# Kernel optimization log

Hardware: AMD Instinct MI355X
Metric: run time of the kernel (lower is better)

Reference implementation:

```python
import jax, jax.numpy as jnp
import numpy as np

N_NODES = 100_000
N_EDGES = 1_600_000
HIDDEN = 256
N_LAYERS = 5
N_GRAPHS = 256
NUM_ATOM_TYPE = 120
NUM_CHIRALITY = 3
NUM_BOND_TYPE = 6
NUM_BOND_DIR = 3


def setup_inputs() -> dict:
    key = jax.random.key(0)
    ks = jax.random.split(key, 16)
    x = jax.random.randint(ks[0], (N_NODES, 2), 0, 3)
    edge_index = jax.random.randint(ks[1], (2, N_EDGES), 0, N_NODES)
    edge_attr = jax.random.randint(ks[2], (N_EDGES, 2), 0, 3)
    batch = jnp.sort(jax.random.randint(ks[3], (N_NODES,), 0, N_GRAPHS))
    # embedding tables (xavier-uniform-ish scale)
    def emb(k, n, d):
        a = np.sqrt(6.0 / (n + d))
        return jax.random.uniform(k, (n, d), jnp.float32, -a, a)
    xe1 = emb(ks[4], NUM_ATOM_TYPE, HIDDEN)
    xe2 = emb(ks[5], NUM_CHIRALITY, HIDDEN)
    ee1 = emb(ks[6], NUM_BOND_TYPE, HIDDEN)
    ee2 = emb(ks[7], NUM_BOND_DIR, HIDDEN)
    s = 1.0 / np.sqrt(HIDDEN)
    W1 = jax.random.uniform(ks[8], (N_LAYERS, HIDDEN, HIDDEN), jnp.float32, -s, s)
    b1 = jax.random.uniform(ks[9], (N_LAYERS, HIDDEN), jnp.float32, -s, s)
    W2 = jax.random.uniform(ks[10], (N_LAYERS, HIDDEN, HIDDEN), jnp.float32, -s, s)
    b2 = jax.random.uniform(ks[11], (N_LAYERS, HIDDEN), jnp.float32, -s, s)
    return {"x": x, "edge_index": edge_index, "edge_attr": edge_attr, "batch": batch,
            "xe1": xe1, "xe2": xe2, "ee1": ee1, "ee2": ee2,
            "W1": W1, "b1": b1, "W2": W2, "b2": b2}


def reference(x, edge_index, edge_attr, batch, xe1, xe2, ee1, ee2, W1, b1, W2, b2):
    # node / edge input embeddings (sum of two lookups)
    z = xe1[x[:, 0]] + xe2[x[:, 1]]                      # [N, H]
    e = ee1[edge_attr[:, 0]] + ee2[edge_attr[:, 1]]      # [E, H]
    src, dst = edge_index[0], edge_index[1]
    for l in range(N_LAYERS):
        # GINEConv: nn((1+eps)*x_i + sum_j relu(x_j + e_ij)), eps = 0
        msg = jax.nn.relu(z[src] + e)                    # [E, H]
        agg = jax.ops.segment_sum(msg, dst, num_segments=N_NODES)
        h = z + agg                                      # (1+0)*x + aggr
        h = jax.nn.relu(h @ W1[l] + b1[l]) @ W2[l] + b2[l]
        z = jax.nn.relu(h)                               # outer relu in GIN.forward
    # global mean pool over graphs
    sums = jax.ops.segment_sum(z, batch, num_segments=N_GRAPHS)      # [G, H]
    cnts = jax.ops.segment_sum(jnp.ones((z.shape[0], 1), z.dtype), batch, num_segments=N_GRAPHS)
    g = sums / jnp.maximum(cnts, 1.0)
    # dropout p=0.0 -> identity
    return (z, g)
```

## Files before the change

kernel.cpp:

```cpp
#include <hip/hip_runtime.h>
#include <hip/hip_bf16.h>

#define HID 256
#define NCODES 18
#define SCAN_CHUNK 2048
#define LROW 264

typedef _Float16 h8_t __attribute__((ext_vector_type(8)));
typedef _Float16 h4_t __attribute__((ext_vector_type(4)));
typedef float f4_t __attribute__((ext_vector_type(4)));

__global__ void etab_kernel(const float* __restrict__ ee1, const float* __restrict__ ee2,
                            _Float16* __restrict__ etab) {
    int t = blockIdx.x;
    int c = threadIdx.x;
    etab[t * HID + c] = (_Float16)(ee1[(t / 3) * HID + c] + ee2[(t % 3) * HID + c]);
}

__global__ __launch_bounds__(256) void embed_kernel(const int* __restrict__ x,
                                                    const float* __restrict__ xe1,
                                                    const float* __restrict__ xe2,
                                                    _Float16* __restrict__ zh, int N) {
    int node = blockIdx.x * 4 + (threadIdx.x >> 6);
    int lane = threadIdx.x & 63;
    if (node >= N) return;
    int a0 = x[node * 2 + 0];
    int a1 = x[node * 2 + 1];
    const float4 u = *(const float4*)(xe1 + (size_t)a0 * HID + lane * 4);
    const float4 v = *(const float4*)(xe2 + (size_t)a1 * HID + lane * 4);
    h4_t r;
    r.x = (_Float16)(u.x + v.x); r.y = (_Float16)(u.y + v.y);
    r.z = (_Float16)(u.z + v.z); r.w = (_Float16)(u.w + v.w);
    *(h4_t*)(zh + (size_t)node * HID + lane * 4) = r;
}

__global__ __launch_bounds__(256) void prep_w(const float* __restrict__ W,
                                              _Float16* __restrict__ Wt) {
    __shared__ float t[32][33];
    int m = blockIdx.z;
    int tx = threadIdx.x & 31, ty = threadIdx.x >> 5;
    const float* Wm = W + (size_t)m * HID * HID;
    _Float16* Wtm = Wt + (size_t)m * HID * HID;
    int k0 = blockIdx.x * 32, n0 = blockIdx.y * 32;
#pragma unroll
    for (int j = 0; j < 4; ++j) { int r = ty + j * 8; t[r][tx] = Wm[(k0 + r) * HID + n0 + tx]; }
    __syncthreads();
#pragma unroll
    for (int j = 0; j < 4; ++j) { int r = ty + j * 8; Wtm[(size_t)(n0 + r) * HID + k0 + tx] = (_Float16)t[tx][r]; }
}

__global__ void hist_kernel(const int* __restrict__ ei, int E, int* __restrict__ deg) {
    int i = blockIdx.x * 256 + threadIdx.x;
    if (i < E) atomicAdd(&deg[ei[E + i]], 1);
}

__global__ __launch_bounds__(256) void scan_partial(const int* __restrict__ deg, int n,
                                                    int* __restrict__ psum) {
    __shared__ int red[256];
    int base = blockIdx.x * SCAN_CHUNK;
    int s = 0;
    for (int i = threadIdx.x; i < SCAN_CHUNK; i += 256) {
        int idx = base + i;
        if (idx < n) s += deg[idx];
    }
    red[threadIdx.x] = s;
    __syncthreads();
    for (int off = 128; off > 0; off >>= 1) {
        if (threadIdx.x < off) red[threadIdx.x] += red[threadIdx.x + off];
        __syncthreads();
    }
    if (threadIdx.x == 0) psum[blockIdx.x] = red[0];
}

__global__ void scan_sums(int* psum, int nchunks) {
    if (blockIdx.x == 0 && threadIdx.x == 0) {
        int acc = 0;
        for (int i = 0; i < nchunks; i++) { int v = psum[i]; psum[i] = acc; acc += v; }
    }
}

__global__ __launch_bounds__(256) void scan_apply(const int* __restrict__ deg, int n,
                                                  const int* __restrict__ psum,
                                                  int* __restrict__ row_start,
                                                  int* __restrict__ cursor, int E) {
    __shared__ int tmp[256];
    int tid = threadIdx.x;
    int base = blockIdx.x * SCAN_CHUNK;
    int tb = base + tid * 8;
    int loc[8];
    int s = 0;
    for (int j = 0; j < 8; j++) {
        loc[j] = s;
        int idx = tb + j;
        if (idx < n) s += deg[idx];
    }
    tmp[tid] = s;
    __syncthreads();
    for (int off = 1; off < 256; off <<= 1) {
        int v = 0;
        if (tid >= off) v = tmp[tid - off];
        __syncthreads();
        if (tid >= off) tmp[tid] += v;
        __syncthreads();
    }
    int excl = tmp[tid] - s + psum[blockIdx.x];
    for (int j = 0; j < 8; j++) {
        int idx = tb + j;
        if (idx < n) {
            int v = excl + loc[j];
            row_start[idx] = v;
            cursor[idx] = v;
        }
    }
    if (blockIdx.x == 0 && tid == 0) row_start[n] = E;
}

__global__ void fill_kernel(const int* __restrict__ ei, const int* __restrict__ ea, int E,
                            int* __restrict__ cursor, unsigned* __restrict__ csr) {
    int i = blockIdx.x * 256 + threadIdx.x;
    if (i >= E) return;
    int dst = ei[E + i];
    int src = ei[i];
    int code = ea[i * 2] * 3 + ea[i * 2 + 1];
    int p = atomicAdd(&cursor[dst], 1);
    csr[p] = (unsigned)src | ((unsigned)code << 20);
}

__global__ __launch_bounds__(256) void agg_kernel(const _Float16* __restrict__ zh,
                                                  const int* __restrict__ row_start,
                                                  const unsigned* __restrict__ csr,
                                                  const _Float16* __restrict__ etab,
                                                  _Float16* __restrict__ h0h, int N) {
    int tid = threadIdx.x;
    int node = blockIdx.x * 8 + (tid >> 5);
    int l32 = tid & 31;
    if (node >= N) return;
    h8_t self = *(const h8_t*)(zh + (size_t)node * HID + l32 * 8);
    float acc[8];
#pragma unroll
    for (int j = 0; j < 8; ++j) acc[j] = (float)self[j];
    int s = row_start[node];
    int e = row_start[node + 1];
    int i = s;
    for (; i + 2 <= e; i += 2) {
        unsigned p0 = csr[i], p1 = csr[i + 1];
        h8_t z0 = *(const h8_t*)(zh + (size_t)(p0 & 0xFFFFF) * HID + l32 * 8);
        h8_t e0 = *(const h8_t*)(etab + (size_t)(p0 >> 20) * HID + l32 * 8);
        h8_t z1 = *(const h8_t*)(zh + (size_t)(p1 & 0xFFFFF) * HID + l32 * 8);
        h8_t e1 = *(const h8_t*)(etab + (size_t)(p1 >> 20) * HID + l32 * 8);
#pragma unroll
        for (int j = 0; j < 8; ++j) {
            acc[j] += fmaxf((float)z0[j] + (float)e0[j], 0.f);
            acc[j] += fmaxf((float)z1[j] + (float)e1[j], 0.f);
        }
    }
    if (i < e) {
        unsigned p0 = csr[i];
        h8_t z0 = *(const h8_t*)(zh + (size_t)(p0 & 0xFFFFF) * HID + l32 * 8);
        h8_t e0 = *(const h8_t*)(etab + (size_t)(p0 >> 20) * HID + l32 * 8);
#pragma unroll
        for (int j = 0; j < 8; ++j) acc[j] += fmaxf((float)z0[j] + (float)e0[j], 0.f);
    }
    h8_t o;
#pragma unroll
    for (int j = 0; j < 8; ++j) o[j] = (_Float16)acc[j];
    *(h8_t*)(h0h + (size_t)node * HID + l32 * 8) = o;
}

__global__ __launch_bounds__(256, 2) void mlp_fused(const _Float16* __restrict__ A,
                                                    const _Float16* __restrict__ Wt1,
                                                    const float* __restrict__ b1,
                                                    const _Float16* __restrict__ Wt2,
                                                    const float* __restrict__ b2,
                                                    _Float16* __restrict__ outh,
                                                    float* __restrict__ outf,
                                                    int M, int writef) {
    __shared__ _Float16 As[64 * LROW];
    __shared__ _Float16 Ys[64 * LROW];
    int tid = threadIdx.x;
    int lane = tid & 63;
    int w = tid >> 6;
    int row0 = blockIdx.x * 64;
    const _Float16* Ab = A + (size_t)row0 * HID;

#pragma unroll
    for (int it = 0; it < 8; ++it) {
        int c = it * 256 + tid;
        int row = c >> 5, cir = c & 31;
        h8_t v = *(const h8_t*)(Ab + row * HID + cir * 8);
        *(h8_t*)(As + row * LROW + cir * 8) = v;
    }
    __syncthreads();

    int wc = w * 64;
    int l16 = lane & 15;
    int lq = lane >> 4;

    {
        f4_t acc[4][4] = {};
#pragma unroll
        for (int ks = 0; ks < 8; ++ks) {
            h8_t a[4], b[4];
#pragma unroll
            for (int mi = 0; mi < 4; ++mi)
                a[mi] = *(const h8_t*)(As + (mi * 16 + l16) * LROW + (ks * 4 + lq) * 8);
#pragma unroll
            for (int ni = 0; ni < 4; ++ni)
                b[ni] = *(const h8_t*)(Wt1 + (size_t)(wc + ni * 16 + l16) * HID + ks * 32 + lq * 8);
#pragma unroll
            for (int mi = 0; mi < 4; ++mi)
#pragma unroll
                for (int ni = 0; ni < 4; ++ni)
                    acc[mi][ni] = __builtin_amdgcn_mfma_f32_16x16x32_f16(a[mi], b[ni], acc[mi][ni], 0, 0, 0);
        }
#pragma unroll
        for (int ni = 0; ni < 4; ++ni) {
            int col = wc + ni * 16 + l16;
            float bv = b1[col];
#pragma unroll
            for (int mi = 0; mi < 4; ++mi)
#pragma unroll
                for (int r = 0; r < 4; ++r) {
                    int rr = mi * 16 + lq * 4 + r;
                    Ys[rr * LROW + col] = (_Float16)fmaxf(acc[mi][ni][r] + bv, 0.f);
                }
        }
    }
    __syncthreads();

    {
        f4_t acc[4][4] = {};
#pragma unroll
        for (int ks = 0; ks < 8; ++ks) {
            h8_t a[4], b[4];
#pragma unroll
            for (int mi = 0; mi < 4; ++mi)
                a[mi] = *(const h8_t*)(Ys + (mi * 16 + l16) * LROW + (ks * 4 + lq) * 8);
#pragma unroll
            for (int ni = 0; ni < 4; ++ni)
                b[ni] = *(const h8_t*)(Wt2 + (size_t)(wc + ni * 16 + l16) * HID + ks * 32 + lq * 8);
#pragma unroll
            for (int mi = 0; mi < 4; ++mi)
#pragma unroll
                for (int ni = 0; ni < 4; ++ni)
                    acc[mi][ni] = __builtin_amdgcn_mfma_f32_16x16x32_f16(a[mi], b[ni], acc[mi][ni], 0, 0, 0);
        }
#pragma unroll
        for (int ni = 0; ni < 4; ++ni) {
            int col = wc + ni * 16 + l16;
            float bv = b2[col];
#pragma unroll
            for (int mi = 0; mi < 4; ++mi)
#pragma unroll
                for (int r = 0; r < 4; ++r) {
                    int rr = mi * 16 + lq * 4 + r;
                    As[rr * LROW + col] = (_Float16)fmaxf(acc[mi][ni][r] + bv, 0.f);
                }
        }
    }
    __syncthreads();

#pragma unroll
    for (int it = 0; it < 8; ++it) {
        int c = it * 256 + tid;
        int row = c >> 5, cir = c & 31;
        int grow = row0 + row;
        if (grow < M) {
            h8_t v = *(const h8_t*)(As + row * LROW + cir * 8);
            *(h8_t*)(outh + (size_t)grow * HID + cir * 8) = v;
            if (writef) {
                f4_t f0, f1;
#pragma unroll
                for (int j = 0; j < 4; ++j) { f0[j] = (float)v[j]; f1[j] = (float)v[j + 4]; }
                *(f4_t*)(outf + (size_t)grow * HID + cir * 8) = f0;
                *(f4_t*)(outf + (size_t)grow * HID + cir * 8 + 4) = f1;
            }
        }
    }
}

__global__ __launch_bounds__(1024) void pool_kernel(const _Float16* __restrict__ zh,
                                                    const int* __restrict__ batch, int N,
                                                    float* __restrict__ g) {
    __shared__ float red[32 * 32 * 8];
    int gid = blockIdx.x;
    int lo = 0, hi = N;
    while (lo < hi) { int mid = (lo + hi) >> 1; if (batch[mid] < gid) lo = mid + 1; else hi = mid; }
    int start = lo;
    int lo2 = start, hi2 = N;
    while (lo2 < hi2) { int mid = (lo2 + hi2) >> 1; if (batch[mid] < gid + 1) lo2 = mid + 1; else hi2 = mid; }
    int end = lo2;
    int cnt = end - start;

    int r = threadIdx.x >> 5;
    int ch = threadIdx.x & 31;
    float acc[8] = {};
    for (int row = start + r; row < end; row += 32) {
        h8_t v = *(const h8_t*)(zh + (size_t)row * HID + ch * 8);
#pragma unroll
        for (int j = 0; j < 8; ++j) acc[j] += (float)v[j];
    }
    float* slot = red + (r * 32 + ch) * 8;
#pragma unroll
    for (int j = 0; j < 8; ++j) slot[j] = acc[j];
    __syncthreads();
    for (int off = 16; off > 0; off >>= 1) {
        if (r < off) {
            const float* o = red + ((r + off) * 32 + ch) * 8;
#pragma unroll
            for (int j = 0; j < 8; ++j) { acc[j] += o[j]; slot[j] = acc[j]; }
        }
        __syncthreads();
    }
    if (r == 0) {
        float inv = 1.0f / fmaxf((float)cnt, 1.0f);
#pragma unroll
        for (int j = 0; j < 8; ++j) g[(size_t)gid * HID + ch * 8 + j] = acc[j] * inv;
    }
}

extern "C" void kernel_launch(void* const* d_in, const int* in_sizes, int n_in,
                              void* d_out, int out_size, void* d_ws, size_t ws_size,
                              hipStream_t stream) {
    const int* x = (const int*)d_in[0];
    const int* ei = (const int*)d_in[1];
    const int* ea = (const int*)d_in[2];
    const int* batch = (const int*)d_in[3];
    const float* xe1 = (const float*)d_in[4];
    const float* xe2 = (const float*)d_in[5];
    const float* ee1 = (const float*)d_in[6];
    const float* ee2 = (const float*)d_in[7];
    const float* W1 = (const float*)d_in[8];
    const float* b1 = (const float*)d_in[9];
    const float* W2 = (const float*)d_in[10];
    const float* b2 = (const float*)d_in[11];

    int N = in_sizes[0] / 2;
    int E = in_sizes[1] / 2;
    int G = out_size / HID - N;
    int Np = ((N + 127) / 128) * 128;
    int nbm = (N + 63) / 64;

    float* z = (float*)d_out;
    float* gout = z + (size_t)N * HID;

    char* w = (char*)d_ws;
    _Float16* h0h = (_Float16*)w;  w += (size_t)Np * HID * 2;
    _Float16* zh  = (_Float16*)w;  w += (size_t)Np * HID * 2;
    _Float16* Wt1 = (_Float16*)w;  w += (size_t)5 * HID * HID * 2;
    _Float16* Wt2 = (_Float16*)w;  w += (size_t)5 * HID * HID * 2;
    _Float16* etabh = (_Float16*)w; w += (size_t)NCODES * HID * 2;
    int* deg = (int*)w;       w += (size_t)N * 4;
    int* row_start = (int*)w; w += (size_t)(N + 1) * 4;
    int* cursor = (int*)w;    w += (size_t)N * 4;
    int* psum = (int*)w;      w += 64 * 4;
    unsigned* csr = (unsigned*)w;

    hipMemsetAsync(deg, 0, (size_t)N * 4, stream);
    etab_kernel<<<NCODES, HID, 0, stream>>>(ee1, ee2, etabh);
    embed_kernel<<<(N + 3) / 4, 256, 0, stream>>>(x, xe1, xe2, zh, N);
    prep_w<<<dim3(8, 8, 5), 256, 0, stream>>>(W1, Wt1);
    prep_w<<<dim3(8, 8, 5), 256, 0, stream>>>(W2, Wt2);
    hist_kernel<<<(E + 255) / 256, 256, 0, stream>>>(ei, E, deg);
    int nchunks = (N + SCAN_CHUNK - 1) / SCAN_CHUNK;
    scan_partial<<<nchunks, 256, 0, stream>>>(deg, N, psum);
    scan_sums<<<1, 1, 0, stream>>>(psum, nchunks);
    scan_apply<<<nchunks, 256, 0, stream>>>(deg, N, psum, row_start, cursor, E);
    fill_kernel<<<(E + 255) / 256, 256, 0, stream>>>(ei, ea, E, cursor, csr);

    for (int l = 0; l < 5; l++) {
        agg_kernel<<<(N + 7) / 8, 256, 0, stream>>>(zh, row_start, csr, etabh, h0h, N);
        mlp_fused<<<nbm, 256, 0, stream>>>(h0h, Wt1 + (size_t)l * HID * HID,
                                           b1 + (size_t)l * HID,
                                           Wt2 + (size_t)l * HID * HID,
                                           b2 + (size_t)l * HID,
                                           zh, z, N, (l == 4) ? 1 : 0);
    }
    pool_kernel<<<G, 1024, 0, stream>>>(zh, batch, N, gout);
}
```

Baseline: 1.280 ms.

## Bucket CSR build, LDS edge table with packed-half aggregation, 512-thread MLP

CSR construction now runs in two passes: edges are first scattered into 128-node buckets, then each bucket is placed into the final CSR by one block, which localizes the per-destination atomics and writes. The aggregation kernel caches the 18-entry edge-embedding table in shared memory, processes four nodes per half-wave with 4-way unrolled gathers, and does the add and relu in packed fp16 before accumulating in fp32. The MLP kernel moves to 512 threads with eight waves splitting both rows and columns, plus an extra barrier before overwriting As. The risks are reduced precision from summing four fp16 messages before the fp32 accumulate, and the packing limits src to 17 bits and code to 5 bits.

```diff
diff --git a/kernel.cpp b/kernel.cpp
--- a/kernel.cpp
+++ b/kernel.cpp
@@ -5,6 +5,7 @@
 #define NCODES 18
 #define SCAN_CHUNK 2048
 #define LROW 264
+#define BSH 7
 
 typedef _Float16 h8_t __attribute__((ext_vector_type(8)));
 typedef _Float16 h4_t __attribute__((ext_vector_type(4)));
@@ -115,15 +116,39 @@
     if (blockIdx.x == 0 && tid == 0) row_start[n] = E;
 }
 
-__global__ void fill_kernel(const int* __restrict__ ei, const int* __restrict__ ea, int E,
-                            int* __restrict__ cursor, unsigned* __restrict__ csr) {
+__global__ void init_bcur(const int* __restrict__ row_start, int* __restrict__ bcur, int nb) {
+    int b = blockIdx.x * 256 + threadIdx.x;
+    if (b < nb) bcur[b] = row_start[b << BSH];
+}
+
+__global__ void bucket_scatter(const int* __restrict__ ei, const int* __restrict__ ea, int E,
+                               int* __restrict__ bcur, unsigned* __restrict__ tmp) {
     int i = blockIdx.x * 256 + threadIdx.x;
     if (i >= E) return;
     int dst = ei[E + i];
     int src = ei[i];
     int code = ea[i * 2] * 3 + ea[i * 2 + 1];
-    int p = atomicAdd(&cursor[dst], 1);
-    csr[p] = (unsigned)src | ((unsigned)code << 20);
+    int b = dst >> BSH;
+    int p = atomicAdd(&bcur[b], 1);
+    tmp[p] = (unsigned)src | ((unsigned)code << 17) | ((unsigned)(dst & 127) << 22);
+}
+
+__global__ __launch_bounds__(256) void bucket_fill(const int* __restrict__ row_start,
+                                                   const unsigned* __restrict__ tmp,
+                                                   int* __restrict__ cursor,
+                                                   unsigned* __restrict__ csr, int N) {
+    int b = blockIdx.x;
+    int lo = b << BSH;
+    int hi = lo + (1 << BSH);
+    if (hi > N) hi = N;
+    int base = row_start[lo];
+    int cnt = row_start[hi] - base;
+    for (int i = threadIdx.x; i < cnt; i += 256) {
+        unsigned e = tmp[base + i];
+        int dst = lo + ((e >> 22) & 127);
+        int pos = atomicAdd(&cursor[dst], 1);
+        csr[pos] = (e & 0x1FFFF) | (((e >> 17) & 31) << 20);
+    }
 }
 
 __global__ __launch_bounds__(256) void agg_kernel(const _Float16* __restrict__ zh,
@@ -131,50 +156,69 @@
                                                   const unsigned* __restrict__ csr,
                                                   const _Float16* __restrict__ etab,
                                                   _Float16* __restrict__ h0h, int N) {
+    __shared__ _Float16 et[NCODES * HID];
     int tid = threadIdx.x;
-    int node = blockIdx.x * 8 + (tid >> 5);
+    for (int c = tid; c < NCODES * 32; c += 256)
+        *(h8_t*)(et + c * 8) = *(const h8_t*)(etab + c * 8);
+    __syncthreads();
+
+    int w = tid >> 6;
     int l32 = tid & 31;
-    if (node >= N) return;
-    h8_t self = *(const h8_t*)(zh + (size_t)node * HID + l32 * 8);
-    float acc[8];
-#pragma unroll
-    for (int j = 0; j < 8; ++j) acc[j] = (float)self[j];
-    int s = row_start[node];
-    int e = row_start[node + 1];
-    int i = s;
-    for (; i + 2 <= e; i += 2) {
-        unsigned p0 = csr[i], p1 = csr[i + 1];
-        h8_t z0 = *(const h8_t*)(zh + (size_t)(p0 & 0xFFFFF) * HID + l32 * 8);
-        h8_t e0 = *(const h8_t*)(etab + (size_t)(p0 >> 20) * HID + l32 * 8);
-        h8_t z1 = *(const h8_t*)(zh + (size_t)(p1 & 0xFFFFF) * HID + l32 * 8);
-        h8_t e1 = *(const h8_t*)(etab + (size_t)(p1 >> 20) * HID + l32 * 8);
-#pragma unroll
-        for (int j = 0; j < 8; ++j) {
-            acc[j] += fmaxf((float)z0[j] + (float)e0[j], 0.f);
-            acc[j] += fmaxf((float)z1[j] + (float)e1[j], 0.f);
-        }
-    }
-    if (i < e) {
-        unsigned p0 = csr[i];
-        h8_t z0 = *(const h8_t*)(zh + (size_t)(p0 & 0xFFFFF) * HID + l32 * 8);
-        h8_t e0 = *(const h8_t*)(etab + (size_t)(p0 >> 20) * HID + l32 * 8);
-#pragma unroll
-        for (int j = 0; j < 8; ++j) acc[j] += fmaxf((float)z0[j] + (float)e0[j], 0.f);
-    }
-    h8_t o;
-#pragma unroll
-    for (int j = 0; j < 8; ++j) o[j] = (_Float16)acc[j];
-    *(h8_t*)(h0h + (size_t)node * HID + l32 * 8) = o;
-}
-
-__global__ __launch_bounds__(256, 2) void mlp_fused(const _Float16* __restrict__ A,
-                                                    const _Float16* __restrict__ Wt1,
-                                                    const float* __restrict__ b1,
-                                                    const _Float16* __restrict__ Wt2,
-                                                    const float* __restrict__ b2,
-                                                    _Float16* __restrict__ outh,
-                                                    float* __restrict__ outf,
-                                                    int M, int writef) {
+    int half = (tid >> 5) & 1;
+    int base = blockIdx.x * 32 + w * 8;
+    const h8_t hz = {};
+
+    for (int t = 0; t < 4; ++t) {
+        int node = base + t * 2 + half;
+        if (node >= N) continue;
+        h8_t self = *(const h8_t*)(zh + (size_t)node * HID + l32 * 8);
+        float acc[8];
+#pragma unroll
+        for (int j = 0; j < 8; ++j) acc[j] = (float)self[j];
+        int s = row_start[node];
+        int e = row_start[node + 1];
+        int i = s;
+        for (; i + 4 <= e; i += 4) {
+            unsigned p0 = csr[i], p1 = csr[i + 1], p2 = csr[i + 2], p3 = csr[i + 3];
+            h8_t z0 = *(const h8_t*)(zh + (size_t)(p0 & 0xFFFFF) * HID + l32 * 8);
+            h8_t z1 = *(const h8_t*)(zh + (size_t)(p1 & 0xFFFFF) * HID + l32 * 8);
+            h8_t z2 = *(const h8_t*)(zh + (size_t)(p2 & 0xFFFFF) * HID + l32 * 8);
+            h8_t z3 = *(const h8_t*)(zh + (size_t)(p3 & 0xFFFFF) * HID + l32 * 8);
+            h8_t e0 = *(const h8_t*)(et + (p0 >> 20) * HID + l32 * 8);
+            h8_t e1 = *(const h8_t*)(et + (p1 >> 20) * HID + l32 * 8);
+            h8_t e2 = *(const h8_t*)(et + (p2 >> 20) * HID + l32 * 8);
+            h8_t e3 = *(const h8_t*)(et + (p3 >> 20) * HID + l32 * 8);
+            h8_t m0 = __builtin_elementwise_max(z0 + e0, hz);
+            h8_t m1 = __builtin_elementwise_max(z1 + e1, hz);
+            h8_t m2 = __builtin_elementwise_max(z2 + e2, hz);
+            h8_t m3 = __builtin_elementwise_max(z3 + e3, hz);
+            h8_t sm = (m0 + m1) + (m2 + m3);
+#pragma unroll
+            for (int j = 0; j < 8; ++j) acc[j] += (float)sm[j];
+        }
+        for (; i < e; ++i) {
+            unsigned p0 = csr[i];
+            h8_t z0 = *(const h8_t*)(zh + (size_t)(p0 & 0xFFFFF) * HID + l32 * 8);
+            h8_t e0 = *(const h8_t*)(et + (p0 >> 20) * HID + l32 * 8);
+            h8_t m0 = __builtin_elementwise_max(z0 + e0, hz);
+#pragma unroll
+            for (int j = 0; j < 8; ++j) acc[j] += (float)m0[j];
+        }
+        h8_t o;
+#pragma unroll
+        for (int j = 0; j < 8; ++j) o[j] = (_Float16)acc[j];
+        *(h8_t*)(h0h + (size_t)node * HID + l32 * 8) = o;
+    }
+}
+
+__global__ __launch_bounds__(512, 4) void mlp_kernel(const _Float16* __restrict__ A,
+                                                     const _Float16* __restrict__ Wt1,
+                                                     const float* __restrict__ b1,
+                                                     const _Float16* __restrict__ Wt2,
+                                                     const float* __restrict__ b2,
+                                                     _Float16* __restrict__ outh,
+                                                     float* __restrict__ outf,
+                                                     int M, int writef) {
     __shared__ _Float16 As[64 * LROW];
     __shared__ _Float16 Ys[64 * LROW];
     int tid = threadIdx.x;
@@ -184,31 +228,31 @@
     const _Float16* Ab = A + (size_t)row0 * HID;
 
 #pragma unroll
-    for (int it = 0; it < 8; ++it) {
-        int c = it * 256 + tid;
+    for (int it = 0; it < 4; ++it) {
+        int c = it * 512 + tid;
         int row = c >> 5, cir = c & 31;
-        h8_t v = *(const h8_t*)(Ab + row * HID + cir * 8);
-        *(h8_t*)(As + row * LROW + cir * 8) = v;
-    }
-    __syncthreads();
-
-    int wc = w * 64;
+        *(h8_t*)(As + row * LROW + cir * 8) = *(const h8_t*)(Ab + row * HID + cir * 8);
+    }
+    __syncthreads();
+
+    int mh = (w >> 2) * 32;
+    int wc = (w & 3) * 64;
     int l16 = lane & 15;
     int lq = lane >> 4;
 
     {
-        f4_t acc[4][4] = {};
+        f4_t acc[2][4] = {};
 #pragma unroll
         for (int ks = 0; ks < 8; ++ks) {
-            h8_t a[4], b[4];
-#pragma unroll
-            for (int mi = 0; mi < 4; ++mi)
-                a[mi] = *(const h8_t*)(As + (mi * 16 + l16) * LROW + (ks * 4 + lq) * 8);
+            h8_t a[2], b[4];
+#pragma unroll
+            for (int mi = 0; mi < 2; ++mi)
+                a[mi] = *(const h8_t*)(As + (mh + mi * 16 + l16) * LROW + (ks * 4 + lq) * 8);
 #pragma unroll
             for (int ni = 0; ni < 4; ++ni)
                 b[ni] = *(const h8_t*)(Wt1 + (size_t)(wc + ni * 16 + l16) * HID + ks * 32 + lq * 8);
 #pragma unroll
-            for (int mi = 0; mi < 4; ++mi)
+            for (int mi = 0; mi < 2; ++mi)
 #pragma unroll
                 for (int ni = 0; ni < 4; ++ni)
                     acc[mi][ni] = __builtin_amdgcn_mfma_f32_16x16x32_f16(a[mi], b[ni], acc[mi][ni], 0, 0, 0);
@@ -218,10 +262,10 @@
             int col = wc + ni * 16 + l16;
             float bv = b1[col];
 #pragma unroll
-            for (int mi = 0; mi < 4; ++mi)
+            for (int mi = 0; mi < 2; ++mi)
 #pragma unroll
                 for (int r = 0; r < 4; ++r) {
-                    int rr = mi * 16 + lq * 4 + r;
+                    int rr = mh + mi * 16 + lq * 4 + r;
                     Ys[rr * LROW + col] = (_Float16)fmaxf(acc[mi][ni][r] + bv, 0.f);
                 }
         }
@@ -229,31 +273,32 @@
     __syncthreads();
 
     {
-        f4_t acc[4][4] = {};
+        f4_t acc[2][4] = {};
 #pragma unroll
         for (int ks = 0; ks < 8; ++ks) {
-            h8_t a[4], b[4];
-#pragma unroll
-            for (int mi = 0; mi < 4; ++mi)
-                a[mi] = *(const h8_t*)(Ys + (mi * 16 + l16) * LROW + (ks * 4 + lq) * 8);
+            h8_t a[2], b[4];
+#pragma unroll
+            for (int mi = 0; mi < 2; ++mi)
+                a[mi] = *(const h8_t*)(Ys + (mh + mi * 16 + l16) * LROW + (ks * 4 + lq) * 8);
 #pragma unroll
             for (int ni = 0; ni < 4; ++ni)
                 b[ni] = *(const h8_t*)(Wt2 + (size_t)(wc + ni * 16 + l16) * HID + ks * 32 + lq * 8);
 #pragma unroll
-            for (int mi = 0; mi < 4; ++mi)
+            for (int mi = 0; mi < 2; ++mi)
 #pragma unroll
                 for (int ni = 0; ni < 4; ++ni)
                     acc[mi][ni] = __builtin_amdgcn_mfma_f32_16x16x32_f16(a[mi], b[ni], acc[mi][ni], 0, 0, 0);
         }
+        __syncthreads();
 #pragma unroll
         for (int ni = 0; ni < 4; ++ni) {
             int col = wc + ni * 16 + l16;
             float bv = b2[col];
 #pragma unroll
-            for (int mi = 0; mi < 4; ++mi)
+            for (int mi = 0; mi < 2; ++mi)
 #pragma unroll
                 for (int r = 0; r < 4; ++r) {
-                    int rr = mi * 16 + lq * 4 + r;
+                    int rr = mh + mi * 16 + lq * 4 + r;
                     As[rr * LROW + col] = (_Float16)fmaxf(acc[mi][ni][r] + bv, 0.f);
                 }
         }
@@ -261,8 +306,8 @@
     __syncthreads();
 
 #pragma unroll
-    for (int it = 0; it < 8; ++it) {
-        int c = it * 256 + tid;
+    for (int it = 0; it < 4; ++it) {
+        int c = it * 512 + tid;
         int row = c >> 5, cir = c & 31;
         int grow = row0 + row;
         if (grow < M) {
@@ -338,8 +383,9 @@
     int N = in_sizes[0] / 2;
     int E = in_sizes[1] / 2;
     int G = out_size / HID - N;
-    int Np = ((N + 127) / 128) * 128;
     int nbm = (N + 63) / 64;
+    int Np = nbm * 64;
+    int nb = (N + (1 << BSH) - 1) >> BSH;
 
     float* z = (float*)d_out;
     float* gout = z + (size_t)N * HID;
@@ -354,7 +400,9 @@
     int* row_start = (int*)w; w += (size_t)(N + 1) * 4;
     int* cursor = (int*)w;    w += (size_t)N * 4;
     int* psum = (int*)w;      w += 64 * 4;
-    unsigned* csr = (unsigned*)w;
+    int* bcur = (int*)w;      w += 1024 * 4;
+    unsigned* csr = (unsigned*)w; w += (size_t)E * 4;
+    unsigned* tmp = (unsigned*)w;
 
     hipMemsetAsync(deg, 0, (size_t)N * 4, stream);
     etab_kernel<<<NCODES, HID, 0, stream>>>(ee1, ee2, etabh);
@@ -366,15 +414,17 @@
     scan_partial<<<nchunks, 256, 0, stream>>>(deg, N, psum);
     scan_sums<<<1, 1, 0, stream>>>(psum, nchunks);
     scan_apply<<<nchunks, 256, 0, stream>>>(deg, N, psum, row_start, cursor, E);
-    fill_kernel<<<(E + 255) / 256, 256, 0, stream>>>(ei, ea, E, cursor, csr);
+    init_bcur<<<(nb + 255) / 256, 256, 0, stream>>>(row_start, bcur, nb);
+    bucket_scatter<<<(E + 255) / 256, 256, 0, stream>>>(ei, ea, E, bcur, tmp);
+    bucket_fill<<<nb, 256, 0, stream>>>(row_start, tmp, cursor, csr, N);
 
     for (int l = 0; l < 5; l++) {
-        agg_kernel<<<(N + 7) / 8, 256, 0, stream>>>(zh, row_start, csr, etabh, h0h, N);
-        mlp_fused<<<nbm, 256, 0, stream>>>(h0h, Wt1 + (size_t)l * HID * HID,
-                                           b1 + (size_t)l * HID,
-                                           Wt2 + (size_t)l * HID * HID,
-                                           b2 + (size_t)l * HID,
-                                           zh, z, N, (l == 4) ? 1 : 0);
+        agg_kernel<<<(N + 31) / 32, 256, 0, stream>>>(zh, row_start, csr, etabh, h0h, N);
+        mlp_kernel<<<nbm, 512, 0, stream>>>(h0h, Wt1 + (size_t)l * HID * HID,
+                                            b1 + (size_t)l * HID,
+                                            Wt2 + (size_t)l * HID * HID,
+                                            b2 + (size_t)l * HID,
+                                            zh, z, N, (l == 4) ? 1 : 0);
     }
     pool_kernel<<<G, 1024, 0, stream>>>(zh, batch, N, gout);
 }
```

New measurement: 1.839 ms. 43.7% more time.
